# Optimization experiments

Hardware: AMD Instinct MI355X
Metric: run time of the kernel (lower is better)

## Reference

```python
import jax, jax.numpy as jnp
import numpy as np

G = (1.0, 1.0)  # Clifford signature g = [1, 1]
MODES1 = 32
MODES2 = 32


def _clifford_kernel_2d(w, g):
    # w: (4, O, Cin, 2*m1, 2*m2); returns (4*O, 4*Cin, 2*m1, 2*m2)
    g0, g1 = g
    k0 = jnp.concatenate([w[0], g0 * w[1], g1 * w[2], -g0 * g1 * w[3]], axis=1)
    k1 = jnp.concatenate([w[1], w[0], -g1 * w[3], g1 * w[2]], axis=1)
    k2 = jnp.concatenate([w[2], g0 * w[3], w[0], -g0 * w[1]], axis=1)
    k3 = jnp.concatenate([w[3], w[2], -w[1], w[0]], axis=1)
    return jnp.concatenate([k0, k1, k2, k3], axis=0)


def _forward(x, weights):
    # x: (B, C, H, W, 4) multivector field
    B, C, H, W, I = x.shape
    m1, m2 = MODES1, MODES2
    # dual-pair complexification: (scalar, e12) and (e1, e2)
    d1 = jax.lax.complex(x[..., 0], x[..., 3])
    d2 = jax.lax.complex(x[..., 1], x[..., 2])
    d1f = jnp.fft.fft2(d1)  # over last two axes (H, W)
    d2f = jnp.fft.fft2(d2)
    # stacked blades in Fourier space: (B, 4*C, H, W)
    mv = jnp.concatenate([d1f.real, d2f.real, d2f.imag, d1f.imag], axis=1)
    # crop low-frequency corner modes into a (2*m1, 2*m2) block
    top = jnp.concatenate([mv[:, :, :m1, :m2], mv[:, :, :m1, -m2:]], axis=-1)
    bot = jnp.concatenate([mv[:, :, -m1:, :m2], mv[:, :, -m1:, -m2:]], axis=-1)
    inp = jnp.concatenate([top, bot], axis=-2)  # (B, 4*C, 2*m1, 2*m2)
    kernel = _clifford_kernel_2d(weights, G)  # (4*O, 4*C, 2*m1, 2*m2)
    out = jnp.einsum('bixy,oixy->boxy', inp, kernel)  # geometric-product mode mix
    O4 = kernel.shape[0]
    # scatter the four corners back into a zero-padded full spectrum
    out_ft = jnp.zeros((B, O4, H, W), dtype=x.dtype)
    out_ft = out_ft.at[:, :, :m1, :m2].set(out[:, :, :m1, :m2])
    out_ft = out_ft.at[:, :, -m1:, :m2].set(out[:, :, -m1:, :m2])
    out_ft = out_ft.at[:, :, :m1, -m2:].set(out[:, :, :m1, -m2:])
    out_ft = out_ft.at[:, :, -m1:, -m2:].set(out[:, :, -m1:, -m2:])
    # (B, 4, O, H, W) -> (B, O, H, W, 4)
    out_ft = out_ft.reshape(B, 4, O4 // 4, H, W).transpose(0, 2, 3, 4, 1)
    od1 = jax.lax.complex(out_ft[..., 0], out_ft[..., 3])
    od2 = jax.lax.complex(out_ft[..., 1], out_ft[..., 2])
    o1 = jnp.fft.ifft2(od1)
    o2 = jnp.fft.ifft2(od2)
    return jnp.stack([o1.real, o2.real, o2.imag, o1.imag], axis=-1)


def setup_inputs() -> dict:
    key = jax.random.key(0)
    kx, kw = jax.random.split(key)
    B, Cin, Cout, H, W = 4, 32, 32, 256, 256
    x = jax.random.normal(kx, (B, Cin, H, W, 4), dtype=jnp.float32)
    scale = 1.0 / (Cin * Cout)
    weights = scale * jax.random.uniform(kw, (4, Cout, Cin, 2 * MODES1, 2 * MODES2), dtype=jnp.float32)
    return {"x": x, "weights": weights}


def reference(x, weights):
    return _forward(x, weights)
```

## Files before the change

### kernel.cpp

```cpp
#include <hip/hip_runtime.h>
#include <hip/hip_fp16.h>
#include <math.h>

#define TWO_PI 6.28318530717958647692f

__device__ __forceinline__ void cmac(float2& a, const float2 b, const float2 c) {
  a.x = fmaf(b.x, c.x, fmaf(-b.y, c.y, a.x));
  a.y = fmaf(b.x, c.y, fmaf(b.y, c.x, a.y));
}
__device__ __forceinline__ __half2 pkh(const float xx, const float yy) {
  return __floats2half2_rn(xx, yy);
}
__device__ __forceinline__ float2 uph(const __half2 h) { return __half22float2(h); }

#define W16_C {1.f, 0.92387953f, 0.70710678f, 0.38268343f, 0.f, -0.38268343f, -0.70710678f, -0.92387953f, -1.f, -0.92387953f, -0.70710678f, -0.38268343f, 0.f, 0.38268343f, 0.70710678f, 0.92387953f}
#define W16_S {0.f, 0.38268343f, 0.70710678f, 0.92387953f, 1.f, 0.92387953f, 0.70710678f, 0.38268343f, 0.f, -0.38268343f, -0.70710678f, -0.92387953f, -1.f, -0.92387953f, -0.70710678f, -0.38268343f}

__device__ __forceinline__ void idft16_p1(const float2* a, const int p1,
                                          float2* X) {
  const float WC[16] = W16_C;
  const float WS[16] = W16_S;
  float2 tt[4];
#pragma unroll
  for (int r1 = 0; r1 < 4; ++r1) {
    const float2 q0 = a[r1], q1 = a[r1 + 4], q2 = a[r1 + 8], q3 = a[r1 + 12];
    const float2 s = make_float2(q0.x + q2.x, q0.y + q2.y);
    const float2 d = make_float2(q0.x - q2.x, q0.y - q2.y);
    const float2 u = make_float2(q1.x + q3.x, q1.y + q3.y);
    const float2 e = make_float2(q1.x - q3.x, q1.y - q3.y);
    float2 in;
    if (p1 == 0)      in = make_float2(s.x + u.x, s.y + u.y);
    else if (p1 == 1) in = make_float2(d.x - e.y, d.y + e.x);
    else if (p1 == 2) in = make_float2(s.x - u.x, s.y - u.y);
    else              in = make_float2(d.x + e.y, d.y - e.x);
    const float wc = WC[(r1 * p1) & 15], ws = WS[(r1 * p1) & 15];
    tt[r1] = make_float2(fmaf(in.x, wc, -in.y * ws), fmaf(in.y, wc, in.x * ws));
  }
  const float2 s = make_float2(tt[0].x + tt[2].x, tt[0].y + tt[2].y);
  const float2 d = make_float2(tt[0].x - tt[2].x, tt[0].y - tt[2].y);
  const float2 u = make_float2(tt[1].x + tt[3].x, tt[1].y + tt[3].y);
  const float2 e = make_float2(tt[1].x - tt[3].x, tt[1].y - tt[3].y);
  X[0] = make_float2(s.x + u.x, s.y + u.y);
  X[1] = make_float2(d.x - e.y, d.y + e.x);
  X[2] = make_float2(s.x - u.x, s.y - u.y);
  X[3] = make_float2(d.x + e.y, d.y - e.x);
}

__global__ __launch_bounds__(256) void f1_dft_h(const float* __restrict__ x,
                                                __half2* __restrict__ G) {
  __shared__ float2 twn[256];
  __shared__ __half2 yf[64][4][20][2];
  __shared__ __half2 dl[2][64][16];
  const int t = threadIdx.x;
  {
    float sv, cv;
    sincosf(-TWO_PI * (float)t * (1.0f / 256.0f), &sv, &cv);
    twn[t] = make_float2(cv, sv);
  }
  const int bid = blockIdx.x;
  const int img = bid >> 4;
  const int w0  = (bid & 15) << 4;
  const float4* __restrict__ xb = (const float4*)x + (size_t)img * 65536 + w0;
  {
    const int wl  = t & 15;
    const int n1g = t >> 4;
#pragma unroll
    for (int ii = 0; ii < 4; ++ii) {
      const int n1 = n1g + (ii << 4);
      const float4 v0 = xb[(size_t)(n1)*256 + wl];
      const float4 v1 = xb[(size_t)(n1 + 64) * 256 + wl];
      const float4 v2 = xb[(size_t)(n1 + 128) * 256 + wl];
      const float4 v3 = xb[(size_t)(n1 + 192) * 256 + wl];
      {
        const float sx = v0.x + v2.x, sy = v0.w + v2.w;
        const float dx = v0.x - v2.x, dy = v0.w - v2.w;
        const float ux = v1.x + v3.x, uy = v1.w + v3.w;
        const float ex = v1.x - v3.x, ey = v1.w - v3.w;
        yf[n1][0][wl][0] = pkh(sx + ux, sy + uy);
        yf[n1][2][wl][0] = pkh(sx - ux, sy - uy);
        yf[n1][1][wl][0] = pkh(dx + ey, dy - ex);
        yf[n1][3][wl][0] = pkh(dx - ey, dy + ex);
      }
      {
        const float sx = v0.y + v2.y, sy = v0.z + v2.z;
        const float dx = v0.y - v2.y, dy = v0.z - v2.z;
        const float ux = v1.y + v3.y, uy = v1.z + v3.z;
        const float ex = v1.y - v3.y, ey = v1.z - v3.z;
        yf[n1][0][wl][1] = pkh(sx + ux, sy + uy);
        yf[n1][2][wl][1] = pkh(sx - ux, sy - uy);
        yf[n1][1][wl][1] = pkh(dx + ey, dy - ex);
        yf[n1][3][wl][1] = pkh(dx - ey, dy + ex);
      }
    }
  }
  __syncthreads();
  const int wl = t & 15;
  const int kb = t >> 4;
  const int r  = kb & 3;
  float2 a0[16], a1[16];
#pragma unroll
  for (int c = 0; c < 16; ++c) {
    a0[c] = make_float2(0.f, 0.f);
    a1[c] = make_float2(0.f, 0.f);
  }
  int idx = 0;
#pragma unroll
  for (int n1 = 0; n1 < 64; ++n1) {
    const float2 tv = twn[idx];
    const float2 hv = *reinterpret_cast<const float2*>(&yf[n1][r][wl][0]);
    const float2 y0 = uph(__builtin_bit_cast(__half2, hv.x));
    const float2 y1 = uph(__builtin_bit_cast(__half2, hv.y));
    cmac(a0[n1 & 15], y0, tv);
    cmac(a1[n1 & 15], y1, tv);
    idx = (idx + kb) & 255;
  }
  const float WC[16] = W16_C;
  const float WS[16] = W16_S;
  float2 D0 = make_float2(0.f, 0.f), D1 = D0, D2 = D0, D3 = D0;
  float2 E0 = D0, E1 = D0, E2 = D0, E3 = D0;
#pragma unroll
  for (int c = 0; c < 16; ++c) {
    const float cc = WC[c], ss = WS[c];
    const float cc2 = WC[(2 * c) & 15], ss2 = WS[(2 * c) & 15];
    {
      const float2 a = a0[c];
      D0.x += a.x;                         D0.y += a.y;
      D1.x = fmaf(a.x, cc,  fmaf( a.y, ss,  D1.x));
      D1.y = fmaf(a.y, cc,  fmaf(-a.x, ss,  D1.y));
      D2.x = fmaf(a.x, cc2, fmaf(-a.y, ss2, D2.x));
      D2.y = fmaf(a.y, cc2, fmaf( a.x, ss2, D2.y));
      D3.x = fmaf(a.x, cc,  fmaf(-a.y, ss,  D3.x));
      D3.y = fmaf(a.y, cc,  fmaf( a.x, ss,  D3.y));
    }
    {
      const float2 a = a1[c];
      E0.x += a.x;                         E0.y += a.y;
      E1.x = fmaf(a.x, cc,  fmaf( a.y, ss,  E1.x));
      E1.y = fmaf(a.y, cc,  fmaf(-a.x, ss,  E1.y));
      E2.x = fmaf(a.x, cc2, fmaf(-a.y, ss2, E2.x));
      E2.y = fmaf(a.y, cc2, fmaf( a.x, ss2, E2.y));
      E3.x = fmaf(a.x, cc,  fmaf(-a.y, ss,  E3.x));
      E3.y = fmaf(a.y, cc,  fmaf( a.x, ss,  E3.y));
    }
  }
  dl[0][kb][wl]      = pkh(D0.x, D0.y);
  dl[0][kb + 16][wl] = pkh(D1.x, D1.y);
  dl[0][kb + 32][wl] = pkh(D2.x, D2.y);
  dl[0][kb + 48][wl] = pkh(D3.x, D3.y);
  dl[1][kb][wl]      = pkh(E0.x, E0.y);
  dl[1][kb + 16][wl] = pkh(E1.x, E1.y);
  dl[1][kb + 32][wl] = pkh(E2.x, E2.y);
  dl[1][kb + 48][wl] = pkh(E3.x, E3.y);
  __syncthreads();
  const __half2* __restrict__ dfl = &dl[0][0][0];
#pragma unroll
  for (int i = 0; i < 8; ++i) {
    const int flat = t + (i << 8);
    const int dual = flat >> 10, kx = (flat >> 4) & 63, w = flat & 15;
    const size_t row = (size_t)(img * 2 + dual) * 64 + kx;
    G[row * 256 + w0 + w] = dfl[flat];
  }
}

__global__ __launch_bounds__(256) void f2_dft_w(const __half2* __restrict__ G,
                                                __half2* __restrict__ mi) {
  __shared__ float2 twn[256];
  __shared__ float2 yf[16][65][4];
  const int t = threadIdx.x;
  {
    float sv, cv;
    sincosf(-TWO_PI * (float)t * (1.0f / 256.0f), &sv, &cv);
    twn[t] = make_float2(cv, sv);
  }
  const int row0 = blockIdx.x * 16;
  for (int idx = t; idx < 1024; idx += 256) {
    const int tr = idx >> 6, n1 = idx & 63;
    const __half2* __restrict__ Gp = G + (size_t)(row0 + tr) * 256;
    const float2 z0 = uph(Gp[n1]), z1 = uph(Gp[n1 + 64]);
    const float2 z2 = uph(Gp[n1 + 128]), z3 = uph(Gp[n1 + 192]);
    const float sx = z0.x + z2.x, sy = z0.y + z2.y;
    const float dx = z0.x - z2.x, dy = z0.y - z2.y;
    const float ux = z1.x + z3.x, uy = z1.y + z3.y;
    const float ex = z1.x - z3.x, ey = z1.y - z3.y;
    yf[tr][n1][0] = make_float2(sx + ux, sy + uy);
    yf[tr][n1][2] = make_float2(sx - ux, sy - uy);
    yf[tr][n1][1] = make_float2(dx + ey, dy - ex);
    yf[tr][n1][3] = make_float2(dx - ey, dy + ex);
  }
  __syncthreads();
  const int kslot = t & 15;
  const int trow  = t >> 4;
  const int r     = kslot & 3;
  float2 acc[16];
#pragma unroll
  for (int c = 0; c < 16; ++c) acc[c] = make_float2(0.f, 0.f);
  int idx = 0;
#pragma unroll
  for (int n1 = 0; n1 < 64; ++n1) {
    const float2 tv = twn[idx];
    const float2 yv = yf[trow][n1][r];
    cmac(acc[n1 & 15], yv, tv);
    idx = (idx + kslot) & 255;
  }
  const float WC[16] = W16_C;
  const float WS[16] = W16_S;
  float2 D[4];
  D[0] = make_float2(0.f, 0.f); D[1] = D[0]; D[2] = D[0]; D[3] = D[0];
#pragma unroll
  for (int c = 0; c < 16; ++c) {
    const float2 a = acc[c];
    const float cc = WC[c], ss = WS[c];
    const float cc2 = WC[(2 * c) & 15], ss2 = WS[(2 * c) & 15];
    D[0].x += a.x;                        D[0].y += a.y;
    D[1].x = fmaf(a.x, cc,  fmaf( a.y, ss,  D[1].x));
    D[1].y = fmaf(a.y, cc,  fmaf(-a.x, ss,  D[1].y));
    D[2].x = fmaf(a.x, cc2, fmaf(-a.y, ss2, D[2].x));
    D[2].y = fmaf(a.y, cc2, fmaf( a.x, ss2, D[2].y));
    D[3].x = fmaf(a.x, cc,  fmaf(-a.y, ss,  D[3].x));
    D[3].y = fmaf(a.y, cc,  fmaf( a.x, ss,  D[3].y));
  }
  const int row  = row0 + trow;
  const int kx   = row & 63;
  const int dual = (row >> 6) & 1;
  const int bc   = row >> 7;
  const int b = bc >> 5, cc = bc & 31;
#pragma unroll
  for (int m = 0; m < 4; ++m) {
    const int kyi = kslot + (m << 4);
    mi[((size_t)((b * 2 + dual) * 32 + cc)) * 4096 + kx * 64 + kyi] =
        pkh(D[m].x, D[m].y);
  }
}

__global__ __launch_bounds__(512) void ein_k(const __half2* __restrict__ mi,
                                             const float* __restrict__ wgt,
                                             __half2* __restrict__ mo) {
  __shared__ float si[4][128][16];
  const int t = threadIdx.x;
  const int bid = blockIdx.x;
  const int m0 = (bid >> 1) << 4;
  const int oh = bid & 1;
  for (int idx = t; idx < 4096; idx += 512) {
    const int q = idx & 15, c = (idx >> 4) & 31, dual = (idx >> 9) & 1, b = idx >> 10;
    const float2 f = uph(mi[((size_t)((b * 2 + dual) * 32 + c)) * 4096 + m0 + q]);
    if (dual == 0) { si[b][c][q] = f.x;      si[b][96 + c][q] = f.y; }
    else           { si[b][32 + c][q] = f.x; si[b][64 + c][q] = f.y; }
  }
  __syncthreads();
  const int q  = t & 15;
  const int o  = oh * 16 + ((t >> 4) & 15);
  const int ch = t >> 8;
  const int c0 = ch << 4;
  const float* __restrict__ wb = wgt + (size_t)o * 131072 + m0 + q;
  float acc[4][4];
#pragma unroll
  for (int b = 0; b < 4; ++b)
#pragma unroll
    for (int r = 0; r < 4; ++r) acc[b][r] = 0.f;
  float wA[4], wB[4];
#pragma unroll
  for (int j = 0; j < 4; ++j) wA[j] = wb[(size_t)j * 4194304 + (size_t)c0 * 4096];
#pragma unroll
  for (int j = 0; j < 4; ++j) wB[j] = wb[(size_t)j * 4194304 + (size_t)(c0 + 1) * 4096];
#pragma unroll 1
  for (int c = c0; c < c0 + 16; ++c) {
    float wv[4];
#pragma unroll
    for (int j = 0; j < 4; ++j) { wv[j] = wA[j]; wA[j] = wB[j]; }
    if (c + 2 < c0 + 16) {
#pragma unroll
      for (int j = 0; j < 4; ++j)
        wB[j] = wb[(size_t)j * 4194304 + (size_t)(c + 2) * 4096];
    }
#pragma unroll
    for (int b = 0; b < 4; ++b) {
      const float iv0 = si[b][c][q];
      const float iv1 = si[b][32 + c][q];
      const float iv2 = si[b][64 + c][q];
      const float iv3 = si[b][96 + c][q];
      acc[b][0] += wv[0] * iv0 + wv[1] * iv1 + wv[2] * iv2 - wv[3] * iv3;
      acc[b][1] += wv[1] * iv0 + wv[0] * iv1 - wv[3] * iv2 + wv[2] * iv3;
      acc[b][2] += wv[2] * iv0 + wv[3] * iv1 + wv[0] * iv2 - wv[1] * iv3;
      acc[b][3] += wv[3] * iv0 + wv[2] * iv1 - wv[1] * iv2 + wv[0] * iv3;
    }
  }
  __syncthreads();
  float* __restrict__ red = &si[0][0][0];
  if (ch == 1) {
    const int tt = t & 255;
#pragma unroll
    for (int b = 0; b < 4; ++b)
#pragma unroll
      for (int r = 0; r < 4; ++r) red[tt * 17 + b * 4 + r] = acc[b][r];
  }
  __syncthreads();
  if (ch == 0) {
#pragma unroll
    for (int b = 0; b < 4; ++b)
#pragma unroll
      for (int r = 0; r < 4; ++r) acc[b][r] += red[t * 17 + b * 4 + r];
#pragma unroll
    for (int b = 0; b < 4; ++b) {
      mo[((size_t)((b * 2 + 0) * 32 + o)) * 4096 + m0 + q] = pkh(acc[b][0], acc[b][3]);
      mo[((size_t)((b * 2 + 1) * 32 + o)) * 4096 + m0 + q] = pkh(acc[b][1], acc[b][2]);
    }
  }
}

__global__ __launch_bounds__(256) void i1_idft_w(const __half2* __restrict__ mo,
                                                 __half2* __restrict__ T) {
  __shared__ float2 twc[256];
  __shared__ float2 srow[16][66];
  const int t = threadIdx.x;
  {
    float sv, cv;
    sincosf(TWO_PI * (float)t * (1.0f / 256.0f), &sv, &cv);
    twc[t] = make_float2(cv, sv);
  }
  const int row0 = blockIdx.x * 16;
  for (int idx = t; idx < 1024; idx += 256) {
    const int tr = idx >> 6, ky = idx & 63;
    const int row = row0 + tr;
    const int kx = row & 63;
    const int dual = (row >> 6) & 1;
    const int bo = row >> 7;
    const int b = bo >> 5, o = bo & 31;
    srow[tr][ky] =
        uph(mo[((size_t)((b * 2 + dual) * 32 + o)) * 4096 + kx * 64 + ky]);
  }
  __syncthreads();
  const int n1   = t & 15;
  const int trow = t >> 4;
  float2 a[16];
#pragma unroll
  for (int c = 0; c < 16; ++c) a[c] = make_float2(0.f, 0.f);
  int idx = 0;
#pragma unroll
  for (int kyi = 0; kyi < 64; ++kyi) {
    if (kyi == 32) idx = (idx + 192 * n1) & 255;
    cmac(a[kyi & 15], srow[trow][kyi], twc[idx]);
    idx = (idx + n1) & 255;
  }
  const int row = row0 + trow;
  __half2* __restrict__ Tp = T + (size_t)row * 256;
#pragma unroll
  for (int p1 = 0; p1 < 4; ++p1) {
    float2 X[4];
    idft16_p1(a, p1, X);
#pragma unroll
    for (int p2 = 0; p2 < 4; ++p2)
      Tp[n1 + 16 * (p1 + 4 * p2)] = pkh(X[p2].x, X[p2].y);
  }
}

__global__ __launch_bounds__(256) void i2_idft_h(const __half2* __restrict__ T,
                                                 float* __restrict__ out) {
  __shared__ float2 twc[256];
  __shared__ float2 Tl[2][64][16];
  const int t = threadIdx.x;
  {
    float sv, cv;
    sincosf(TWO_PI * (float)t * (1.0f / 256.0f), &sv, &cv);
    twc[t] = make_float2(cv, sv);
  }
  const int bid = blockIdx.x;
  const int bo = bid >> 4;
  const int w0 = (bid & 15) << 4;
  const __half2* __restrict__ Tp = T + (size_t)bo * 32768;
  for (int idx = t; idx < 2048; idx += 256) {
    const int ww = idx & 15, kxi = (idx >> 4) & 63, dual = idx >> 10;
    Tl[dual][kxi][ww] = uph(Tp[((size_t)dual * 64 + kxi) * 256 + w0 + ww]);
  }
  __syncthreads();
  const int wl = t & 15;
  const int n1 = t >> 4;
  float2 a0[16], a1[16];
#pragma unroll
  for (int c = 0; c < 16; ++c) {
    a0[c] = make_float2(0.f, 0.f);
    a1[c] = make_float2(0.f, 0.f);
  }
  int idx = 0;
#pragma unroll
  for (int kxi = 0; kxi < 64; ++kxi) {
    if (kxi == 32) idx = (idx + 192 * n1) & 255;
    const float2 tv = twc[idx];
    cmac(a0[kxi & 15], Tl[0][kxi][wl], tv);
    cmac(a1[kxi & 15], Tl[1][kxi][wl], tv);
    idx = (idx + n1) & 255;
  }
  const float sc = 1.0f / 65536.0f;
  float4* __restrict__ op = (float4*)out + (size_t)bo * 65536 + w0 + wl;
#pragma unroll
  for (int p1 = 0; p1 < 4; ++p1) {
    float2 X0[4], X1[4];
    idft16_p1(a0, p1, X0);
    idft16_p1(a1, p1, X1);
#pragma unroll
    for (int p2 = 0; p2 < 4; ++p2) {
      const int h = n1 + 16 * (p1 + 4 * p2);
      op[(size_t)h * 256] = make_float4(X0[p2].x * sc, X1[p2].x * sc,
                                        X1[p2].y * sc, X0[p2].y * sc);
    }
  }
}

extern "C" void kernel_launch(void* const* d_in, const int* in_sizes, int n_in,
                              void* d_out, int out_size, void* d_ws, size_t ws_size,
                              hipStream_t stream) {
  const float* x = (const float*)d_in[0];
  const float* wgt = (const float*)d_in[1];
  float* out = (float*)d_out;
  __half2* G  = (__half2*)d_ws;
  __half2* mi = G + 4194304;
  __half2* mo = mi + 1048576;

  hipLaunchKernelGGL(f1_dft_h, dim3(2048), dim3(256), 0, stream, x, G);
  hipLaunchKernelGGL(f2_dft_w, dim3(1024), dim3(256), 0, stream, G, mi);
  hipLaunchKernelGGL(ein_k,    dim3(512),  dim3(512), 0, stream, mi, wgt, mo);
  hipLaunchKernelGGL(i1_idft_w, dim3(1024), dim3(256), 0, stream, mo, G);
  hipLaunchKernelGGL(i2_idft_h, dim3(2048), dim3(256), 0, stream, G, out);
}
```

Measured before the change: 126.3 us.

## Rebalance thread mapping in forward H-DFT and einsum kernels with vectorized IO

The forward H-direction DFT kernel now uses 512 threads, with each thread handling one dual component instead of two. This halves the per-thread accumulator registers, and the output staging reuses the input shared buffer, which lowers LDS use and allows a single float4 store per thread. The einsum kernel drops the split-channel reduction through shared memory. Each of its 256 threads now owns one batch and four modes, using float4 weight and shared loads and packed half stores. The trade-off is more work per thread in the einsum and fewer threads per einsum block, which may reduce latency hiding for the weight loads.

```diff
diff --git a/kernel.cpp b/kernel.cpp
--- a/kernel.cpp
+++ b/kernel.cpp
@@ -12,6 +12,21 @@
   return __floats2half2_rn(xx, yy);
 }
 __device__ __forceinline__ float2 uph(const __half2 h) { return __half22float2(h); }
+
+#define FMA4(a, b, v)                 \
+  {                                   \
+    a.x = fmaf(b.x, v.x, a.x);        \
+    a.y = fmaf(b.y, v.y, a.y);        \
+    a.z = fmaf(b.z, v.z, a.z);        \
+    a.w = fmaf(b.w, v.w, a.w);        \
+  }
+#define FMS4(a, b, v)                 \
+  {                                   \
+    a.x = fmaf(-b.x, v.x, a.x);       \
+    a.y = fmaf(-b.y, v.y, a.y);       \
+    a.z = fmaf(-b.z, v.z, a.z);       \
+    a.w = fmaf(-b.w, v.w, a.w);       \
+  }
 
 #define W16_C {1.f, 0.92387953f, 0.70710678f, 0.38268343f, 0.f, -0.38268343f, -0.70710678f, -0.92387953f, -1.f, -0.92387953f, -0.70710678f, -0.38268343f, 0.f, 0.38268343f, 0.70710678f, 0.92387953f}
 #define W16_S {0.f, 0.38268343f, 0.70710678f, 0.92387953f, 1.f, 0.92387953f, 0.70710678f, 0.38268343f, 0.f, -0.38268343f, -0.70710678f, -0.92387953f, -1.f, -0.92387953f, -0.70710678f, -0.38268343f}
@@ -46,13 +61,12 @@
   X[3] = make_float2(d.x + e.y, d.y - e.x);
 }
 
-__global__ __launch_bounds__(256) void f1_dft_h(const float* __restrict__ x,
+__global__ __launch_bounds__(512) void f1_dft_h(const float* __restrict__ x,
                                                 __half2* __restrict__ G) {
   __shared__ float2 twn[256];
-  __shared__ __half2 yf[64][4][20][2];
-  __shared__ __half2 dl[2][64][16];
+  __shared__ __align__(16) __half2 yf[64][4][17][2];
   const int t = threadIdx.x;
-  {
+  if (t < 256) {
     float sv, cv;
     sincosf(-TWO_PI * (float)t * (1.0f / 256.0f), &sv, &cv);
     twn[t] = make_float2(cv, sv);
@@ -61,105 +75,80 @@
   const int img = bid >> 4;
   const int w0  = (bid & 15) << 4;
   const float4* __restrict__ xb = (const float4*)x + (size_t)img * 65536 + w0;
-  {
-    const int wl  = t & 15;
-    const int n1g = t >> 4;
-#pragma unroll
-    for (int ii = 0; ii < 4; ++ii) {
-      const int n1 = n1g + (ii << 4);
-      const float4 v0 = xb[(size_t)(n1)*256 + wl];
-      const float4 v1 = xb[(size_t)(n1 + 64) * 256 + wl];
-      const float4 v2 = xb[(size_t)(n1 + 128) * 256 + wl];
-      const float4 v3 = xb[(size_t)(n1 + 192) * 256 + wl];
-      {
-        const float sx = v0.x + v2.x, sy = v0.w + v2.w;
-        const float dx = v0.x - v2.x, dy = v0.w - v2.w;
-        const float ux = v1.x + v3.x, uy = v1.w + v3.w;
-        const float ex = v1.x - v3.x, ey = v1.w - v3.w;
-        yf[n1][0][wl][0] = pkh(sx + ux, sy + uy);
-        yf[n1][2][wl][0] = pkh(sx - ux, sy - uy);
-        yf[n1][1][wl][0] = pkh(dx + ey, dy - ex);
-        yf[n1][3][wl][0] = pkh(dx - ey, dy + ex);
-      }
-      {
-        const float sx = v0.y + v2.y, sy = v0.z + v2.z;
-        const float dx = v0.y - v2.y, dy = v0.z - v2.z;
-        const float ux = v1.y + v3.y, uy = v1.z + v3.z;
-        const float ex = v1.y - v3.y, ey = v1.z - v3.z;
-        yf[n1][0][wl][1] = pkh(sx + ux, sy + uy);
-        yf[n1][2][wl][1] = pkh(sx - ux, sy - uy);
-        yf[n1][1][wl][1] = pkh(dx + ey, dy - ex);
-        yf[n1][3][wl][1] = pkh(dx - ey, dy + ex);
-      }
+#pragma unroll
+  for (int i = 0; i < 2; ++i) {
+    const int idxs = t + (i << 9);
+    const int n1 = idxs >> 4, wl = idxs & 15;
+    const float4 v0 = xb[(size_t)(n1)*256 + wl];
+    const float4 v1 = xb[(size_t)(n1 + 64) * 256 + wl];
+    const float4 v2 = xb[(size_t)(n1 + 128) * 256 + wl];
+    const float4 v3 = xb[(size_t)(n1 + 192) * 256 + wl];
+    {
+      const float sx = v0.x + v2.x, sy = v0.w + v2.w;
+      const float dx = v0.x - v2.x, dy = v0.w - v2.w;
+      const float ux = v1.x + v3.x, uy = v1.w + v3.w;
+      const float ex = v1.x - v3.x, ey = v1.w - v3.w;
+      yf[n1][0][wl][0] = pkh(sx + ux, sy + uy);
+      yf[n1][2][wl][0] = pkh(sx - ux, sy - uy);
+      yf[n1][1][wl][0] = pkh(dx + ey, dy - ex);
+      yf[n1][3][wl][0] = pkh(dx - ey, dy + ex);
     }
-  }
-  __syncthreads();
-  const int wl = t & 15;
-  const int kb = t >> 4;
-  const int r  = kb & 3;
-  float2 a0[16], a1[16];
-#pragma unroll
-  for (int c = 0; c < 16; ++c) {
-    a0[c] = make_float2(0.f, 0.f);
-    a1[c] = make_float2(0.f, 0.f);
-  }
+    {
+      const float sx = v0.y + v2.y, sy = v0.z + v2.z;
+      const float dx = v0.y - v2.y, dy = v0.z - v2.z;
+      const float ux = v1.y + v3.y, uy = v1.z + v3.z;
+      const float ex = v1.y - v3.y, ey = v1.z - v3.z;
+      yf[n1][0][wl][1] = pkh(sx + ux, sy + uy);
+      yf[n1][2][wl][1] = pkh(sx - ux, sy - uy);
+      yf[n1][1][wl][1] = pkh(dx + ey, dy - ex);
+      yf[n1][3][wl][1] = pkh(dx - ey, dy + ex);
+    }
+  }
+  __syncthreads();
+  const int wl   = t & 15;
+  const int dual = (t >> 4) & 1;
+  const int kb   = t >> 5;
+  const int r    = kb & 3;
+  float2 a[16];
+#pragma unroll
+  for (int c = 0; c < 16; ++c) a[c] = make_float2(0.f, 0.f);
   int idx = 0;
 #pragma unroll
   for (int n1 = 0; n1 < 64; ++n1) {
     const float2 tv = twn[idx];
-    const float2 hv = *reinterpret_cast<const float2*>(&yf[n1][r][wl][0]);
-    const float2 y0 = uph(__builtin_bit_cast(__half2, hv.x));
-    const float2 y1 = uph(__builtin_bit_cast(__half2, hv.y));
-    cmac(a0[n1 & 15], y0, tv);
-    cmac(a1[n1 & 15], y1, tv);
+    const float2 yv = uph(yf[n1][r][wl][dual]);
+    cmac(a[n1 & 15], yv, tv);
     idx = (idx + kb) & 255;
   }
   const float WC[16] = W16_C;
   const float WS[16] = W16_S;
   float2 D0 = make_float2(0.f, 0.f), D1 = D0, D2 = D0, D3 = D0;
-  float2 E0 = D0, E1 = D0, E2 = D0, E3 = D0;
 #pragma unroll
   for (int c = 0; c < 16; ++c) {
+    const float2 av = a[c];
     const float cc = WC[c], ss = WS[c];
     const float cc2 = WC[(2 * c) & 15], ss2 = WS[(2 * c) & 15];
-    {
-      const float2 a = a0[c];
-      D0.x += a.x;                         D0.y += a.y;
-      D1.x = fmaf(a.x, cc,  fmaf( a.y, ss,  D1.x));
-      D1.y = fmaf(a.y, cc,  fmaf(-a.x, ss,  D1.y));
-      D2.x = fmaf(a.x, cc2, fmaf(-a.y, ss2, D2.x));
-      D2.y = fmaf(a.y, cc2, fmaf( a.x, ss2, D2.y));
-      D3.x = fmaf(a.x, cc,  fmaf(-a.y, ss,  D3.x));
-      D3.y = fmaf(a.y, cc,  fmaf( a.x, ss,  D3.y));
-    }
-    {
-      const float2 a = a1[c];
-      E0.x += a.x;                         E0.y += a.y;
-      E1.x = fmaf(a.x, cc,  fmaf( a.y, ss,  E1.x));
-      E1.y = fmaf(a.y, cc,  fmaf(-a.x, ss,  E1.y));
-      E2.x = fmaf(a.x, cc2, fmaf(-a.y, ss2, E2.x));
-      E2.y = fmaf(a.y, cc2, fmaf( a.x, ss2, E2.y));
-      E3.x = fmaf(a.x, cc,  fmaf(-a.y, ss,  E3.x));
-      E3.y = fmaf(a.y, cc,  fmaf( a.x, ss,  E3.y));
-    }
-  }
-  dl[0][kb][wl]      = pkh(D0.x, D0.y);
-  dl[0][kb + 16][wl] = pkh(D1.x, D1.y);
-  dl[0][kb + 32][wl] = pkh(D2.x, D2.y);
-  dl[0][kb + 48][wl] = pkh(D3.x, D3.y);
-  dl[1][kb][wl]      = pkh(E0.x, E0.y);
-  dl[1][kb + 16][wl] = pkh(E1.x, E1.y);
-  dl[1][kb + 32][wl] = pkh(E2.x, E2.y);
-  dl[1][kb + 48][wl] = pkh(E3.x, E3.y);
+    D0.x += av.x;                        D0.y += av.y;
+    D1.x = fmaf(av.x, cc,  fmaf( av.y, ss,  D1.x));
+    D1.y = fmaf(av.y, cc,  fmaf(-av.x, ss,  D1.y));
+    D2.x = fmaf(av.x, cc2, fmaf(-av.y, ss2, D2.x));
+    D2.y = fmaf(av.y, cc2, fmaf( av.x, ss2, D2.y));
+    D3.x = fmaf(av.x, cc,  fmaf(-av.y, ss,  D3.x));
+    D3.y = fmaf(av.y, cc,  fmaf( av.x, ss,  D3.y));
+  }
+  __syncthreads();
+  __half2(*dl)[64][16] = reinterpret_cast<__half2(*)[64][16]>(&yf[0][0][0][0]);
+  dl[dual][kb][wl]      = pkh(D0.x, D0.y);
+  dl[dual][kb + 16][wl] = pkh(D1.x, D1.y);
+  dl[dual][kb + 32][wl] = pkh(D2.x, D2.y);
+  dl[dual][kb + 48][wl] = pkh(D3.x, D3.y);
   __syncthreads();
   const __half2* __restrict__ dfl = &dl[0][0][0];
-#pragma unroll
-  for (int i = 0; i < 8; ++i) {
-    const int flat = t + (i << 8);
-    const int dual = flat >> 10, kx = (flat >> 4) & 63, w = flat & 15;
-    const size_t row = (size_t)(img * 2 + dual) * 64 + kx;
-    G[row * 256 + w0 + w] = dfl[flat];
-  }
+  const int flat = t << 2;
+  const int wq = flat & 15, kx = (flat >> 4) & 63, dd = flat >> 10;
+  const size_t row = (size_t)(img * 2 + dd) * 64 + kx;
+  *reinterpret_cast<float4*>(&G[row * 256 + w0 + wq]) =
+      *reinterpret_cast<const float4*>(&dfl[flat]);
 }
 
 __global__ __launch_bounds__(256) void f2_dft_w(const __half2* __restrict__ G,
@@ -232,7 +221,7 @@
   }
 }
 
-__global__ __launch_bounds__(512) void ein_k(const __half2* __restrict__ mi,
+__global__ __launch_bounds__(256) void ein_k(const __half2* __restrict__ mi,
                                              const float* __restrict__ wgt,
                                              __half2* __restrict__ mo) {
   __shared__ float si[4][128][16];
@@ -240,71 +229,62 @@
   const int bid = blockIdx.x;
   const int m0 = (bid >> 1) << 4;
   const int oh = bid & 1;
-  for (int idx = t; idx < 4096; idx += 512) {
+  for (int idx = t; idx < 4096; idx += 256) {
     const int q = idx & 15, c = (idx >> 4) & 31, dual = (idx >> 9) & 1, b = idx >> 10;
     const float2 f = uph(mi[((size_t)((b * 2 + dual) * 32 + c)) * 4096 + m0 + q]);
     if (dual == 0) { si[b][c][q] = f.x;      si[b][96 + c][q] = f.y; }
     else           { si[b][32 + c][q] = f.x; si[b][64 + c][q] = f.y; }
   }
   __syncthreads();
-  const int q  = t & 15;
-  const int o  = oh * 16 + ((t >> 4) & 15);
-  const int ch = t >> 8;
-  const int c0 = ch << 4;
-  const float* __restrict__ wb = wgt + (size_t)o * 131072 + m0 + q;
-  float acc[4][4];
-#pragma unroll
-  for (int b = 0; b < 4; ++b)
-#pragma unroll
-    for (int r = 0; r < 4; ++r) acc[b][r] = 0.f;
-  float wA[4], wB[4];
-#pragma unroll
-  for (int j = 0; j < 4; ++j) wA[j] = wb[(size_t)j * 4194304 + (size_t)c0 * 4096];
-#pragma unroll
-  for (int j = 0; j < 4; ++j) wB[j] = wb[(size_t)j * 4194304 + (size_t)(c0 + 1) * 4096];
+  const int qv  = t & 3;
+  const int o16 = (t >> 2) & 15;
+  const int b   = t >> 6;
+  const int o   = oh * 16 + o16;
+  const int q0  = qv << 2;
+  const float* __restrict__ wb = wgt + (size_t)o * 131072 + m0 + q0;
+  float4 acc[4];
+#pragma unroll
+  for (int r = 0; r < 4; ++r) acc[r] = make_float4(0.f, 0.f, 0.f, 0.f);
+  float4 wA[4], wB[4];
+#pragma unroll
+  for (int j = 0; j < 4; ++j)
+    wA[j] = *reinterpret_cast<const float4*>(&wb[(size_t)j * 4194304]);
+#pragma unroll
+  for (int j = 0; j < 4; ++j)
+    wB[j] = *reinterpret_cast<const float4*>(&wb[(size_t)j * 4194304 + 4096]);
 #pragma unroll 1
-  for (int c = c0; c < c0 + 16; ++c) {
-    float wv[4];
+  for (int c = 0; c < 32; ++c) {
+    float4 wv[4];
 #pragma unroll
     for (int j = 0; j < 4; ++j) { wv[j] = wA[j]; wA[j] = wB[j]; }
-    if (c + 2 < c0 + 16) {
+    if (c + 2 < 32) {
 #pragma unroll
       for (int j = 0; j < 4; ++j)
-        wB[j] = wb[(size_t)j * 4194304 + (size_t)(c + 2) * 4096];
+        wB[j] = *reinterpret_cast<const float4*>(
+            &wb[(size_t)j * 4194304 + (size_t)(c + 2) * 4096]);
     }
-#pragma unroll
-    for (int b = 0; b < 4; ++b) {
-      const float iv0 = si[b][c][q];
-      const float iv1 = si[b][32 + c][q];
-      const float iv2 = si[b][64 + c][q];
-      const float iv3 = si[b][96 + c][q];
-      acc[b][0] += wv[0] * iv0 + wv[1] * iv1 + wv[2] * iv2 - wv[3] * iv3;
-      acc[b][1] += wv[1] * iv0 + wv[0] * iv1 - wv[3] * iv2 + wv[2] * iv3;
-      acc[b][2] += wv[2] * iv0 + wv[3] * iv1 + wv[0] * iv2 - wv[1] * iv3;
-      acc[b][3] += wv[3] * iv0 + wv[2] * iv1 - wv[1] * iv2 + wv[0] * iv3;
-    }
-  }
-  __syncthreads();
-  float* __restrict__ red = &si[0][0][0];
-  if (ch == 1) {
-    const int tt = t & 255;
-#pragma unroll
-    for (int b = 0; b < 4; ++b)
-#pragma unroll
-      for (int r = 0; r < 4; ++r) red[tt * 17 + b * 4 + r] = acc[b][r];
-  }
-  __syncthreads();
-  if (ch == 0) {
-#pragma unroll
-    for (int b = 0; b < 4; ++b)
-#pragma unroll
-      for (int r = 0; r < 4; ++r) acc[b][r] += red[t * 17 + b * 4 + r];
-#pragma unroll
-    for (int b = 0; b < 4; ++b) {
-      mo[((size_t)((b * 2 + 0) * 32 + o)) * 4096 + m0 + q] = pkh(acc[b][0], acc[b][3]);
-      mo[((size_t)((b * 2 + 1) * 32 + o)) * 4096 + m0 + q] = pkh(acc[b][1], acc[b][2]);
-    }
-  }
+    const float4 iv0 = *reinterpret_cast<const float4*>(&si[b][c][q0]);
+    const float4 iv1 = *reinterpret_cast<const float4*>(&si[b][32 + c][q0]);
+    const float4 iv2 = *reinterpret_cast<const float4*>(&si[b][64 + c][q0]);
+    const float4 iv3 = *reinterpret_cast<const float4*>(&si[b][96 + c][q0]);
+    FMA4(acc[0], wv[0], iv0); FMA4(acc[0], wv[1], iv1);
+    FMA4(acc[0], wv[2], iv2); FMS4(acc[0], wv[3], iv3);
+    FMA4(acc[1], wv[1], iv0); FMA4(acc[1], wv[0], iv1);
+    FMS4(acc[1], wv[3], iv2); FMA4(acc[1], wv[2], iv3);
+    FMA4(acc[2], wv[2], iv0); FMA4(acc[2], wv[3], iv1);
+    FMA4(acc[2], wv[0], iv2); FMS4(acc[2], wv[1], iv3);
+    FMA4(acc[3], wv[3], iv0); FMA4(acc[3], wv[2], iv1);
+    FMS4(acc[3], wv[1], iv2); FMA4(acc[3], wv[0], iv3);
+  }
+  __half2 h0[4], h1[4];
+  h0[0] = pkh(acc[0].x, acc[3].x); h0[1] = pkh(acc[0].y, acc[3].y);
+  h0[2] = pkh(acc[0].z, acc[3].z); h0[3] = pkh(acc[0].w, acc[3].w);
+  h1[0] = pkh(acc[1].x, acc[2].x); h1[1] = pkh(acc[1].y, acc[2].y);
+  h1[2] = pkh(acc[1].z, acc[2].z); h1[3] = pkh(acc[1].w, acc[2].w);
+  *reinterpret_cast<float4*>(&mo[((size_t)((b * 2 + 0) * 32 + o)) * 4096 + m0 + q0]) =
+      *reinterpret_cast<const float4*>(h0);
+  *reinterpret_cast<float4*>(&mo[((size_t)((b * 2 + 1) * 32 + o)) * 4096 + m0 + q0]) =
+      *reinterpret_cast<const float4*>(h1);
 }
 
 __global__ __launch_bounds__(256) void i1_idft_w(const __half2* __restrict__ mo,
@@ -415,9 +395,9 @@
   __half2* mi = G + 4194304;
   __half2* mo = mi + 1048576;
 
-  hipLaunchKernelGGL(f1_dft_h, dim3(2048), dim3(256), 0, stream, x, G);
+  hipLaunchKernelGGL(f1_dft_h, dim3(2048), dim3(512), 0, stream, x, G);
   hipLaunchKernelGGL(f2_dft_w, dim3(1024), dim3(256), 0, stream, G, mi);
-  hipLaunchKernelGGL(ein_k,    dim3(512),  dim3(512), 0, stream, mi, wgt, mo);
+  hipLaunchKernelGGL(ein_k,    dim3(512),  dim3(256), 0, stream, mi, wgt, mo);
   hipLaunchKernelGGL(i1_idft_w, dim3(1024), dim3(256), 0, stream, mo, G);
   hipLaunchKernelGGL(i2_idft_h, dim3(2048), dim3(256), 0, stream, G, out);
 }
```

Result: no change. 128.8 us (+1.9%).

## Split einsum kernel over 4-way channel chunks with smaller mode tiles

Applied to the files above, without the earlier changes.

The mode-mixing kernel now handles 8 modes per block instead of 16 and splits the input-channel reduction four ways instead of two, doubling the grid to 1024 blocks. The channel loop is unrolled by two, with separate even and odd weight prefetch registers, and the partial sums are combined through a two-stage shared-memory tree reduction. The aim is more parallelism and better latency hiding on the weight stream, at the cost of extra barriers and reduction traffic, and weight loads now coalesce over only 8 consecutive modes.

```diff
diff --git a/kernel.cpp b/kernel.cpp
--- a/kernel.cpp
+++ b/kernel.cpp
@@ -235,70 +235,128 @@
 __global__ __launch_bounds__(512) void ein_k(const __half2* __restrict__ mi,
                                              const float* __restrict__ wgt,
                                              __half2* __restrict__ mo) {
-  __shared__ float si[4][128][16];
+  __shared__ float si[4][128][8];
+  __shared__ float red[2][128][17];
   const int t = threadIdx.x;
   const int bid = blockIdx.x;
-  const int m0 = (bid >> 1) << 4;
+  const int m0 = (bid >> 1) << 3;
   const int oh = bid & 1;
-  for (int idx = t; idx < 4096; idx += 512) {
-    const int q = idx & 15, c = (idx >> 4) & 31, dual = (idx >> 9) & 1, b = idx >> 10;
+  for (int idx = t; idx < 2048; idx += 512) {
+    const int q = idx & 7, c = (idx >> 3) & 31, dual = (idx >> 8) & 1, b = idx >> 9;
     const float2 f = uph(mi[((size_t)((b * 2 + dual) * 32 + c)) * 4096 + m0 + q]);
     if (dual == 0) { si[b][c][q] = f.x;      si[b][96 + c][q] = f.y; }
     else           { si[b][32 + c][q] = f.x; si[b][64 + c][q] = f.y; }
   }
   __syncthreads();
-  const int q  = t & 15;
-  const int o  = oh * 16 + ((t >> 4) & 15);
-  const int ch = t >> 8;
-  const int c0 = ch << 4;
+  const int q   = t & 7;
+  const int o16 = (t >> 3) & 15;
+  const int ch  = t >> 7;
+  const int o   = oh * 16 + o16;
+  const int c0  = ch << 3;
+  const int oq  = o16 * 8 + q;
   const float* __restrict__ wb = wgt + (size_t)o * 131072 + m0 + q;
   float acc[4][4];
 #pragma unroll
   for (int b = 0; b < 4; ++b)
 #pragma unroll
     for (int r = 0; r < 4; ++r) acc[b][r] = 0.f;
-  float wA[4], wB[4];
-#pragma unroll
-  for (int j = 0; j < 4; ++j) wA[j] = wb[(size_t)j * 4194304 + (size_t)c0 * 4096];
-#pragma unroll
-  for (int j = 0; j < 4; ++j) wB[j] = wb[(size_t)j * 4194304 + (size_t)(c0 + 1) * 4096];
+  float wE[4], wO[4];
+#pragma unroll
+  for (int j = 0; j < 4; ++j)
+    wE[j] = wb[(size_t)j * 4194304 + (size_t)c0 * 4096];
+#pragma unroll
+  for (int j = 0; j < 4; ++j)
+    wO[j] = wb[(size_t)j * 4194304 + (size_t)(c0 + 1) * 4096];
 #pragma unroll 1
-  for (int c = c0; c < c0 + 16; ++c) {
-    float wv[4];
-#pragma unroll
-    for (int j = 0; j < 4; ++j) { wv[j] = wA[j]; wA[j] = wB[j]; }
-    if (c + 2 < c0 + 16) {
-#pragma unroll
-      for (int j = 0; j < 4; ++j)
-        wB[j] = wb[(size_t)j * 4194304 + (size_t)(c + 2) * 4096];
-    }
-#pragma unroll
-    for (int b = 0; b < 4; ++b) {
-      const float iv0 = si[b][c][q];
-      const float iv1 = si[b][32 + c][q];
-      const float iv2 = si[b][64 + c][q];
-      const float iv3 = si[b][96 + c][q];
-      acc[b][0] += wv[0] * iv0 + wv[1] * iv1 + wv[2] * iv2 - wv[3] * iv3;
-      acc[b][1] += wv[1] * iv0 + wv[0] * iv1 - wv[3] * iv2 + wv[2] * iv3;
-      acc[b][2] += wv[2] * iv0 + wv[3] * iv1 + wv[0] * iv2 - wv[1] * iv3;
-      acc[b][3] += wv[3] * iv0 + wv[2] * iv1 - wv[1] * iv2 + wv[0] * iv3;
-    }
-  }
-  __syncthreads();
-  float* __restrict__ red = &si[0][0][0];
+  for (int cc = 0; cc < 8; cc += 2) {
+    const int c = c0 + cc;
+    {
+      const float iv0 = si[0][c][q], jv0 = si[1][c][q], kv0 = si[2][c][q], lv0 = si[3][c][q];
+      const float iv1 = si[0][32 + c][q], jv1 = si[1][32 + c][q], kv1 = si[2][32 + c][q], lv1 = si[3][32 + c][q];
+      const float iv2 = si[0][64 + c][q], jv2 = si[1][64 + c][q], kv2 = si[2][64 + c][q], lv2 = si[3][64 + c][q];
+      const float iv3 = si[0][96 + c][q], jv3 = si[1][96 + c][q], kv3 = si[2][96 + c][q], lv3 = si[3][96 + c][q];
+      acc[0][0] += wE[0] * iv0 + wE[1] * iv1 + wE[2] * iv2 - wE[3] * iv3;
+      acc[0][1] += wE[1] * iv0 + wE[0] * iv1 - wE[3] * iv2 + wE[2] * iv3;
+      acc[0][2] += wE[2] * iv0 + wE[3] * iv1 + wE[0] * iv2 - wE[1] * iv3;
+      acc[0][3] += wE[3] * iv0 + wE[2] * iv1 - wE[1] * iv2 + wE[0] * iv3;
+      acc[1][0] += wE[0] * jv0 + wE[1] * jv1 + wE[2] * jv2 - wE[3] * jv3;
+      acc[1][1] += wE[1] * jv0 + wE[0] * jv1 - wE[3] * jv2 + wE[2] * jv3;
+      acc[1][2] += wE[2] * jv0 + wE[3] * jv1 + wE[0] * jv2 - wE[1] * jv3;
+      acc[1][3] += wE[3] * jv0 + wE[2] * jv1 - wE[1] * jv2 + wE[0] * jv3;
+      acc[2][0] += wE[0] * kv0 + wE[1] * kv1 + wE[2] * kv2 - wE[3] * kv3;
+      acc[2][1] += wE[1] * kv0 + wE[0] * kv1 - wE[3] * kv2 + wE[2] * kv3;
+      acc[2][2] += wE[2] * kv0 + wE[3] * kv1 + wE[0] * kv2 - wE[1] * kv3;
+      acc[2][3] += wE[3] * kv0 + wE[2] * kv1 - wE[1] * kv2 + wE[0] * kv3;
+      acc[3][0] += wE[0] * lv0 + wE[1] * lv1 + wE[2] * lv2 - wE[3] * lv3;
+      acc[3][1] += wE[1] * lv0 + wE[0] * lv1 - wE[3] * lv2 + wE[2] * lv3;
+      acc[3][2] += wE[2] * lv0 + wE[3] * lv1 + wE[0] * lv2 - wE[1] * lv3;
+      acc[3][3] += wE[3] * lv0 + wE[2] * lv1 - wE[1] * lv2 + wE[0] * lv3;
+      if (cc + 2 < 8) {
+#pragma unroll
+        for (int j = 0; j < 4; ++j)
+          wE[j] = wb[(size_t)j * 4194304 + (size_t)(c + 2) * 4096];
+      }
+    }
+    {
+      const int c1 = c + 1;
+      const float iv0 = si[0][c1][q], jv0 = si[1][c1][q], kv0 = si[2][c1][q], lv0 = si[3][c1][q];
+      const float iv1 = si[0][32 + c1][q], jv1 = si[1][32 + c1][q], kv1 = si[2][32 + c1][q], lv1 = si[3][32 + c1][q];
+      const float iv2 = si[0][64 + c1][q], jv2 = si[1][64 + c1][q], kv2 = si[2][64 + c1][q], lv2 = si[3][64 + c1][q];
+      const float iv3 = si[0][96 + c1][q], jv3 = si[1][96 + c1][q], kv3 = si[2][96 + c1][q], lv3 = si[3][96 + c1][q];
+      acc[0][0] += wO[0] * iv0 + wO[1] * iv1 + wO[2] * iv2 - wO[3] * iv3;
+      acc[0][1] += wO[1] * iv0 + wO[0] * iv1 - wO[3] * iv2 + wO[2] * iv3;
+      acc[0][2] += wO[2] * iv0 + wO[3] * iv1 + wO[0] * iv2 - wO[1] * iv3;
+      acc[0][3] += wO[3] * iv0 + wO[2] * iv1 - wO[1] * iv2 + wO[0] * iv3;
+      acc[1][0] += wO[0] * jv0 + wO[1] * jv1 + wO[2] * jv2 - wO[3] * jv3;
+      acc[1][1] += wO[1] * jv0 + wO[0] * jv1 - wO[3] * jv2 + wO[2] * jv3;
+      acc[1][2] += wO[2] * jv0 + wO[3] * jv1 + wO[0] * jv2 - wO[1] * jv3;
+      acc[1][3] += wO[3] * jv0 + wO[2] * jv1 - wO[1] * jv2 + wO[0] * jv3;
+      acc[2][0] += wO[0] * kv0 + wO[1] * kv1 + wO[2] * kv2 - wO[3] * kv3;
+      acc[2][1] += wO[1] * kv0 + wO[0] * kv1 - wO[3] * kv2 + wO[2] * kv3;
+      acc[2][2] += wO[2] * kv0 + wO[3] * kv1 + wO[0] * kv2 - wO[1] * kv3;
+      acc[2][3] += wO[3] * kv0 + wO[2] * kv1 - wO[1] * kv2 + wO[0] * kv3;
+      acc[3][0] += wO[0] * lv0 + wO[1] * lv1 + wO[2] * lv2 - wO[3] * lv3;
+      acc[3][1] += wO[1] * lv0 + wO[0] * lv1 - wO[3] * lv2 + wO[2] * lv3;
+      acc[3][2] += wO[2] * lv0 + wO[3] * lv1 + wO[0] * lv2 - wO[1] * lv3;
+      acc[3][3] += wO[3] * lv0 + wO[2] * lv1 - wO[1] * lv2 + wO[0] * lv3;
+      if (cc + 3 < 8) {
+#pragma unroll
+        for (int j = 0; j < 4; ++j)
+          wO[j] = wb[(size_t)j * 4194304 + (size_t)(c + 3) * 4096];
+      }
+    }
+  }
+  __syncthreads();
+  if (ch >= 2) {
+    float* rp = &red[ch - 2][oq][0];
+#pragma unroll
+    for (int b = 0; b < 4; ++b)
+#pragma unroll
+      for (int r = 0; r < 4; ++r) rp[b * 4 + r] = acc[b][r];
+  }
+  __syncthreads();
+  if (ch < 2) {
+    const float* rp = &red[ch][oq][0];
+#pragma unroll
+    for (int b = 0; b < 4; ++b)
+#pragma unroll
+      for (int r = 0; r < 4; ++r) acc[b][r] += rp[b * 4 + r];
+  }
+  __syncthreads();
   if (ch == 1) {
-    const int tt = t & 255;
+    float* rp = &red[0][oq][0];
 #pragma unroll
     for (int b = 0; b < 4; ++b)
 #pragma unroll
-      for (int r = 0; r < 4; ++r) red[tt * 17 + b * 4 + r] = acc[b][r];
+      for (int r = 0; r < 4; ++r) rp[b * 4 + r] = acc[b][r];
   }
   __syncthreads();
   if (ch == 0) {
+    const float* rp = &red[0][oq][0];
 #pragma unroll
     for (int b = 0; b < 4; ++b)
 #pragma unroll
-      for (int r = 0; r < 4; ++r) acc[b][r] += red[t * 17 + b * 4 + r];
+      for (int r = 0; r < 4; ++r) acc[b][r] += rp[b * 4 + r];
 #pragma unroll
     for (int b = 0; b < 4; ++b) {
       mo[((size_t)((b * 2 + 0) * 32 + o)) * 4096 + m0 + q] = pkh(acc[b][0], acc[b][3]);
@@ -417,7 +475,7 @@
 
   hipLaunchKernelGGL(f1_dft_h, dim3(2048), dim3(256), 0, stream, x, G);
   hipLaunchKernelGGL(f2_dft_w, dim3(1024), dim3(256), 0, stream, G, mi);
-  hipLaunchKernelGGL(ein_k,    dim3(512),  dim3(512), 0, stream, mi, wgt, mo);
+  hipLaunchKernelGGL(ein_k,    dim3(1024), dim3(512), 0, stream, mi, wgt, mo);
   hipLaunchKernelGGL(i1_idft_w, dim3(1024), dim3(256), 0, stream, mo, G);
   hipLaunchKernelGGL(i2_idft_h, dim3(2048), dim3(256), 0, stream, G, out);
 }
```

Measured after the change: 148.8 us. +17.7%, slower.
